# Kernel optimization log

Measured on AMD Instinct MI355X. Metric: run time of the kernel, lower is better.

The kernel has to match this reference:

```python
import jax, jax.numpy as jnp
import numpy as np

T, H, I, E, TOPK = 8192, 2048, 4096, 8, 2

def setup_inputs() -> dict:
    key = jax.random.key(0)
    k1, k2, k3, k4 = jax.random.split(key, 4)
    x = jax.random.normal(k1, (T, H), dtype=jnp.float32)
    gate_w = jax.random.normal(k2, (E, H), dtype=jnp.float32) * 0.02
    ws = jax.random.normal(k3, (E, 2 * I, H), dtype=jnp.float32) * 0.02
    w2s = jax.random.normal(k4, (E, H, I), dtype=jnp.float32) * 0.02
    return {"x": x, "gate_w": gate_w, "ws": ws, "w2s": w2s, "top_k": TOPK}

def reference(x, gate_w, ws, w2s, top_k):
    num_tokens = x.shape[0]
    num_experts = ws.shape[0]
    inter = w2s.shape[2]
    # --- router (fused_topk): softmax -> top-k -> renormalize ---
    logits = x @ gate_w.T                       # [T, E]
    probs = jax.nn.softmax(logits, axis=-1)
    topk_w, topk_ids = jax.lax.top_k(probs, top_k)   # [T, K]
    if top_k > 1:
        topk_w = topk_w / jnp.sum(topk_w, axis=-1, keepdims=True)
    # dense combine-weights [E, T]: sum of routing weights per (token, expert)
    tok = jnp.arange(num_tokens)
    cw = jnp.zeros((num_tokens, num_experts), dtype=x.dtype)
    cw = cw.at[tok[:, None], topk_ids].add(topk_w)
    cw = cw.T                                   # [E, T]
    # --- fused_experts: per-expert gated-SiLU MLP, weighted combine ---
    def body(acc, inp):
        e_ws, e_w2, e_cw = inp                  # [2I,H], [H,I], [T]
        gu = x @ e_ws.T                         # [T, 2I]
        g, u = gu[:, :inter], gu[:, inter:]
        h = jax.nn.silu(g) * u                  # SiluAndMul
        out = h @ e_w2.T                        # [T, H]
        return acc + e_cw[:, None] * out, None
    init = jnp.zeros_like(x)
    final, _ = jax.lax.scan(body, init, (ws, w2s, cw))
    return final
```

## Files before the change

kernel.cpp:

```cpp
#include <hip/hip_runtime.h>
#include <hip/hip_fp16.h>
#include <cstdint>
#include <cstddef>

#define TTOK 8192
#define HD   2048
#define ID   4096
#define NE   8
#define NPAIR (TTOK * 2)
#define PADROWS 18432
#define RBMAX 72

typedef _Float16 h8 __attribute__((ext_vector_type(8)));
typedef float    f4 __attribute__((ext_vector_type(4)));

#define VMWAIT(n) asm volatile("s_waitcnt vmcnt(" #n ")" ::: "memory")
#define MEMFENCE  asm volatile("" ::: "memory")
#define BAR()     __builtin_amdgcn_s_barrier()

__device__ __forceinline__ void async_cp16(const void* g, void* l) {
  __builtin_amdgcn_global_load_lds(
      (const __attribute__((address_space(1))) unsigned int*)g,
      (__attribute__((address_space(3))) unsigned int*)l, 16, 0, 0);
}

__device__ __forceinline__ f4 zero4() { f4 z = {0.f, 0.f, 0.f, 0.f}; return z; }

template <bool NT>
__global__ void cvt_kernel(const float* __restrict__ src, _Float16* __restrict__ dst, size_t n) {
  size_t stride = (size_t)gridDim.x * blockDim.x * 8;
  for (size_t i = ((size_t)blockIdx.x * blockDim.x + threadIdx.x) * 8; i < n; i += stride) {
    const float4* s = (const float4*)(src + i);
    float4 a = s[0], b = s[1];
    h8 o;
    o[0] = (_Float16)a.x; o[1] = (_Float16)a.y; o[2] = (_Float16)a.z; o[3] = (_Float16)a.w;
    o[4] = (_Float16)b.x; o[5] = (_Float16)b.y; o[6] = (_Float16)b.z; o[7] = (_Float16)b.w;
    if constexpr (NT) __builtin_nontemporal_store(o, (h8*)(dst + i));
    else *(h8*)(dst + i) = o;
  }
}

__device__ __forceinline__ void cvt_w2_half(const float* __restrict__ w2f,
                                            _Float16* __restrict__ dst,
                                            int kh, int cb, int ncb) {
  const size_t n = (size_t)NE * HD * 2048;
  size_t stride = (size_t)ncb * 512 * 8;
  for (size_t j = ((size_t)cb * 512 + threadIdx.x) * 8; j < n; j += stride) {
    size_t row = j >> 11, ic = j & 2047;
    const float4* s = (const float4*)(w2f + row * ID + (size_t)kh * 2048 + ic);
    float4 a = s[0], b = s[1];
    h8 o;
    o[0] = (_Float16)a.x; o[1] = (_Float16)a.y; o[2] = (_Float16)a.z; o[3] = (_Float16)a.w;
    o[4] = (_Float16)b.x; o[5] = (_Float16)b.y; o[6] = (_Float16)b.z; o[7] = (_Float16)b.w;
    *(h8*)(dst + row * 2048 + ic) = o;
  }
}

__global__ __launch_bounds__(512) void cvt_w2half_kernel(
    const float* __restrict__ w2f, _Float16* __restrict__ dst, int kh) {
  cvt_w2_half(w2f, dst, kh, blockIdx.x, gridDim.x);
}

__global__ __launch_bounds__(256) void gate_kernel(
    const float* __restrict__ x, const float* __restrict__ gw,
    int* __restrict__ counts, int* __restrict__ tids, float* __restrict__ tw,
    _Float16* __restrict__ xh) {
  int lane = threadIdx.x & 63;
  int t = blockIdx.x * 4 + (threadIdx.x >> 6);
  const float* xr = x + (size_t)t * HD;
  _Float16* xhr = xh + (size_t)t * HD;
  float acc[NE];
#pragma unroll
  for (int e = 0; e < NE; e++) acc[e] = 0.f;
  for (int j = lane; j < HD; j += 64) {
    float xv = xr[j];
    xhr[j] = (_Float16)xv;
#pragma unroll
    for (int e = 0; e < NE; e++) acc[e] += xv * gw[e * HD + j];
  }
#pragma unroll
  for (int off = 32; off > 0; off >>= 1) {
#pragma unroll
    for (int e = 0; e < NE; e++) acc[e] += __shfl_xor(acc[e], off, 64);
  }
  if (lane == 0) {
    int e0 = 0; float v0 = acc[0];
#pragma unroll
    for (int e = 1; e < NE; e++) if (acc[e] > v0) { v0 = acc[e]; e0 = e; }
    int e1 = -1; float v1 = -1e30f;
#pragma unroll
    for (int e = 0; e < NE; e++) if (e != e0 && acc[e] > v1) { v1 = acc[e]; e1 = e; }
    float b = __expf(v1 - v0);
    float w0 = 1.f / (1.f + b);
    tids[2 * t] = e0; tids[2 * t + 1] = e1;
    tw[2 * t] = w0;   tw[2 * t + 1] = b * w0;
    atomicAdd(&counts[e0], 1); atomicAdd(&counts[e1], 1);
  }
}

__global__ void scan_kernel(const int* __restrict__ counts, int* __restrict__ offs,
                            int* __restrict__ cursor) {
  if (threadIdx.x == 0 && blockIdx.x == 0) {
    int off = 0;
    for (int e = 0; e < NE; e++) {
      offs[e] = off; cursor[e] = off;
      off += ((counts[e] + 255) >> 8) << 8;
    }
    offs[NE] = off;
  }
}

__global__ void scatter_kernel(const int* __restrict__ tids, const float* __restrict__ tw,
                               int* __restrict__ cursor, int* __restrict__ perm,
                               float* __restrict__ pw, int* __restrict__ pairpos) {
  int t = blockIdx.x * 256 + threadIdx.x;
#pragma unroll
  for (int k = 0; k < 2; k++) {
    int e = tids[2 * t + k];
    int pos = atomicAdd(&cursor[e], 1);
    perm[pos] = t; pw[pos] = tw[2 * t + k];
    pairpos[2 * t + k] = pos;
  }
}

__global__ void padfill_kernel(const int* __restrict__ counts, const int* __restrict__ offs,
                               int* __restrict__ perm) {
  int s = blockIdx.x * 256 + threadIdx.x;
#pragma unroll
  for (int e = 0; e < NE; e++) {
    if (s >= offs[e] + counts[e] && s < offs[e + 1]) perm[s] = -1;
  }
}

#define LA(BB, H) ((BB) * 65536 + (H) * 16384)
#define LB(BB, H) ((BB) * 65536 + 32768 + (H) * 16384)
#define RD(boff) (*(const h8*)(smem + (boff)))

#define LOAD_AF(BB, MH) do { \
  af[0][0] = RD(LA(BB,MH) + amoff + 0*2048 + sa0); \
  af[0][1] = RD(LA(BB,MH) + amoff + 0*2048 + sa1); \
  af[1][0] = RD(LA(BB,MH) + amoff + 1*2048 + sa0); \
  af[1][1] = RD(LA(BB,MH) + amoff + 1*2048 + sa1); \
  af[2][0] = RD(LA(BB,MH) + amoff + 2*2048 + sa0); \
  af[2][1] = RD(LA(BB,MH) + amoff + 2*2048 + sa1); \
  af[3][0] = RD(LA(BB,MH) + amoff + 3*2048 + sa0); \
  af[3][1] = RD(LA(BB,MH) + amoff + 3*2048 + sa1); } while (0)

#define LOAD_BFG(BB) do { \
  bfg[0][0] = RD(LB(BB,0) + bnoff + 0*2048 + sa0); \
  bfg[0][1] = RD(LB(BB,0) + bnoff + 0*2048 + sa1); \
  bfg[1][0] = RD(LB(BB,0) + bnoff + 1*2048 + sa0); \
  bfg[1][1] = RD(LB(BB,0) + bnoff + 1*2048 + sa1); } while (0)

#define LOAD_BFU(BB) do { \
  bfu[0][0] = RD(LB(BB,1) + bnoff + 0*2048 + sa0); \
  bfu[0][1] = RD(LB(BB,1) + bnoff + 0*2048 + sa1); \
  bfu[1][0] = RD(LB(BB,1) + bnoff + 1*2048 + sa0); \
  bfu[1][1] = RD(LB(BB,1) + bnoff + 1*2048 + sa1); } while (0)

#define MM(MH,NH,BF,M,N) \
  acc[MH][NH][M][N] = __builtin_amdgcn_mfma_f32_16x16x32_f16(af[M][0], BF[N][0], acc[MH][NH][M][N], 0, 0, 0); \
  acc[MH][NH][M][N] = __builtin_amdgcn_mfma_f32_16x16x32_f16(af[M][1], BF[N][1], acc[MH][NH][M][N], 0, 0, 0);

#define MFMAQ(MH,NH,BF) do { __builtin_amdgcn_s_setprio(1); \
  MM(MH,NH,BF,0,0) MM(MH,NH,BF,0,1) MM(MH,NH,BF,1,0) MM(MH,NH,BF,1,1) \
  MM(MH,NH,BF,2,0) MM(MH,NH,BF,2,1) MM(MH,NH,BF,3,0) MM(MH,NH,BF,3,1) \
  __builtin_amdgcn_s_setprio(0); } while (0)

#define STG(gp, ldsbyte, kt) do { \
  async_cp16(gp[0] + (size_t)(kt) * 64, smem + (ldsbyte) + (wid * 2 + 0) * 1024 + lane * 16); \
  async_cp16(gp[1] + (size_t)(kt) * 64, smem + (ldsbyte) + (wid * 2 + 1) * 1024 + lane * 16); } while (0)

#define ACC_ZERO() do { \
  _Pragma("unroll") for (int mh = 0; mh < 2; mh++) \
  _Pragma("unroll") for (int nh = 0; nh < 2; nh++) \
  _Pragma("unroll") for (int m = 0; m < 4; m++) \
  _Pragma("unroll") for (int n = 0; n < 2; n++) acc[mh][nh][m][n] = zero4(); } while (0)

#define KLOOP(NI) \
  STG(gA[0], LA(0,0), 0); STG(gA[1], LA(0,1), 0); \
  STG(gB[0], LB(0,0), 0); STG(gB[1], LB(0,1), 0); \
  STG(gA[0], LA(1,0), 1); STG(gB[1], LB(1,1), 1); \
  VMWAIT(4); \
  BAR(); \
  for (int i = 0; i < (NI); ++i) { \
    bool last = (i == (NI) - 1); \
    int kt1 = 2 * i + 1, kt2 = 2 * i + 2, kt3 = 2 * i + 3; \
     \
    MEMFENCE; LOAD_AF(0,0); LOAD_BFG(0); \
    STG(gA[1], LA(1,1), kt1); STG(gB[0], LB(1,0), kt1); \
    BAR(); MEMFENCE; MFMAQ(0,0,bfg); BAR(); \
     \
    MEMFENCE; LOAD_BFU(0); \
    BAR(); MEMFENCE; MFMAQ(0,1,bfu); BAR(); \
     \
    MEMFENCE; LOAD_AF(0,1); \
    if (!last) STG(gA[0], LA(0,0), kt2); \
    BAR(); MEMFENCE; MFMAQ(1,1,bfu); BAR(); \
     \
    MEMFENCE; \
    if (!last) { STG(gB[1], LB(0,1), kt2); VMWAIT(4); } else { VMWAIT(0); } \
    BAR(); MEMFENCE; MFMAQ(1,0,bfg); BAR(); \
     \
    MEMFENCE; LOAD_AF(1,0); LOAD_BFG(1); \
    if (!last) { STG(gA[1], LA(0,1), kt2); STG(gB[0], LB(0,0), kt2); } \
    BAR(); MEMFENCE; MFMAQ(0,0,bfg); BAR(); \
     \
    MEMFENCE; LOAD_BFU(1); \
    BAR(); MEMFENCE; MFMAQ(0,1,bfu); BAR(); \
     \
    MEMFENCE; LOAD_AF(1,1); \
    if (!last) STG(gA[0], LA(1,0), kt3); \
    BAR(); MEMFENCE; MFMAQ(1,1,bfu); BAR(); \
     \
    MEMFENCE; \
    if (!last) { STG(gB[1], LB(1,1), kt3); VMWAIT(4); } \
    BAR(); MEMFENCE; MFMAQ(1,0,bfg); BAR(); \
  }

__device__ __forceinline__ int expert_of(const int* offs, int row0) {
  int e = 0;
#pragma unroll
  for (int k = 1; k < NE; k++) if (offs[k] <= row0) e = k;
  return e;
}

__global__ __launch_bounds__(512, 2) void gemm1_kernel(
    const _Float16* __restrict__ xh, const _Float16* __restrict__ wsh,
    const int* __restrict__ offs, const int* __restrict__ perm,
    _Float16* __restrict__ hb,
    const float* __restrict__ w2f, _Float16* __restrict__ w2h0) {
  int bx = blockIdx.x, gyy = blockIdx.y;
  if (gyy >= RBMAX) {
    cvt_w2_half(w2f, w2h0, 0, (gyy - RBMAX) * 32 + bx, 256);
    return;
  }
  int row0 = gyy << 8;
  if (row0 >= offs[NE]) return;
  int e = expert_of(offs, row0);
  int n0 = bx << 7;

  __shared__ char smem[131072];
  int tid = threadIdx.x, lane = tid & 63, wid = tid >> 6;
  int wm = wid >> 2, wn = wid & 3;
  int lr = lane & 15, ks = lane >> 4;
  int sa0 = lr * 128 + (((ks)     ^ (lr & 7)) << 4);
  int sa1 = lr * 128 + (((ks + 4) ^ (lr & 7)) << 4);
  int amoff = wm * 8192;
  int bnoff = wn * 4096;

  int srow = wid * 16 + (lane >> 3);
  int scol = ((lane & 7) ^ (lane >> 3)) * 8;
  const _Float16* gA[2][2]; const _Float16* gB[2][2];
#pragma unroll
  for (int h = 0; h < 2; h++)
#pragma unroll
    for (int j = 0; j < 2; j++) {
      int r = row0 + h * 128 + srow + j * 8;
      int pv = perm[r]; if (pv < 0) pv = 0;
      gA[h][j] = xh + (size_t)pv * HD + scol;
      gB[h][j] = wsh + ((size_t)e * 2 * ID + (size_t)h * ID + n0 + srow + j * 8) * HD + scol;
    }

  f4 acc[2][2][4][2];
  h8 af[4][2], bfg[2][2], bfu[2][2];
  ACC_ZERO();

  KLOOP(16)

#pragma unroll
  for (int mh = 0; mh < 2; mh++)
#pragma unroll
    for (int m = 0; m < 4; m++)
#pragma unroll
      for (int n = 0; n < 2; n++)
#pragma unroll
        for (int r = 0; r < 4; r++) {
          float g = acc[mh][0][m][n][r], u = acc[mh][1][m][n][r];
          float hv = g / (1.f + __expf(-g)) * u;
          int row = row0 + mh * 128 + wm * 64 + m * 16 + ks * 4 + r;
          int col = n0 + wn * 32 + n * 16 + lr;
          __builtin_nontemporal_store((_Float16)hv, hb + (size_t)row * ID + col);
        }
}

__global__ __launch_bounds__(512, 2) void gemm2_kernel(
    const _Float16* __restrict__ hb, const _Float16* __restrict__ w2h0,
    const _Float16* __restrict__ w2h1, const int* __restrict__ offs,
    _Float16* __restrict__ hb2) {
  int bx = blockIdx.x, gyy = blockIdx.y;
  int row0 = gyy << 8;
  if (row0 >= offs[NE]) return;
  int e = expert_of(offs, row0);
  int n0 = bx << 8;
  int kh = blockIdx.z;
  const _Float16* w2hk = kh ? w2h1 : w2h0;
  size_t k0 = (size_t)kh * 2048;

  __shared__ char smem[131072];
  int tid = threadIdx.x, lane = tid & 63, wid = tid >> 6;
  int wm = wid >> 2, wn = wid & 3;
  int lr = lane & 15, ks = lane >> 4;
  int sa0 = lr * 128 + (((ks)     ^ (lr & 7)) << 4);
  int sa1 = lr * 128 + (((ks + 4) ^ (lr & 7)) << 4);
  int amoff = wm * 8192;
  int bnoff = wn * 4096;

  int srow = wid * 16 + (lane >> 3);
  int scol = ((lane & 7) ^ (lane >> 3)) * 8;
  const _Float16* gA[2][2]; const _Float16* gB[2][2];
#pragma unroll
  for (int h = 0; h < 2; h++)
#pragma unroll
    for (int j = 0; j < 2; j++) {
      gA[h][j] = hb + ((size_t)(row0 + h * 128 + srow + j * 8)) * ID + k0 + scol;
      gB[h][j] = w2hk + ((size_t)e * HD + n0 + h * 128 + srow + j * 8) * 2048 + scol;
    }

  f4 acc[2][2][4][2];
  h8 af[4][2], bfg[2][2], bfu[2][2];
  ACC_ZERO();

  KLOOP(16)

  _Float16* dst = hb2 + (size_t)kh * PADROWS * HD;
#pragma unroll
  for (int mh = 0; mh < 2; mh++)
#pragma unroll
    for (int nh = 0; nh < 2; nh++)
#pragma unroll
      for (int m = 0; m < 4; m++)
#pragma unroll
        for (int n = 0; n < 2; n++)
#pragma unroll
          for (int r = 0; r < 4; r++) {
            int row = row0 + mh * 128 + wm * 64 + m * 16 + ks * 4 + r;
            int col = n0 + nh * 128 + wn * 32 + n * 16 + lr;
            hb2[(size_t)kh * PADROWS * HD + (size_t)row * HD + col] =
                (_Float16)acc[mh][nh][m][n][r];
            (void)dst;
          }
}

__global__ __launch_bounds__(256) void combine_kernel(
    const _Float16* __restrict__ hb2, const int* __restrict__ pairpos,
    const float* __restrict__ pw, float* __restrict__ out) {
  int i = blockIdx.x * 256 + threadIdx.x;
  int t = i >> 8, g = (i & 255) * 8;
  int p0 = pairpos[2 * t], p1 = pairpos[2 * t + 1];
  float w0 = pw[p0], w1 = pw[p1];
  const _Float16* hb2b = hb2 + (size_t)PADROWS * HD;
  h8 a0 = *(const h8*)(hb2  + (size_t)p0 * HD + g);
  h8 a1 = *(const h8*)(hb2b + (size_t)p0 * HD + g);
  h8 b0 = *(const h8*)(hb2  + (size_t)p1 * HD + g);
  h8 b1 = *(const h8*)(hb2b + (size_t)p1 * HD + g);
  f4 o0, o1;
#pragma unroll
  for (int j = 0; j < 4; j++)
    o0[j] = w0 * ((float)a0[j] + (float)a1[j]) + w1 * ((float)b0[j] + (float)b1[j]);
#pragma unroll
  for (int j = 0; j < 4; j++)
    o1[j] = w0 * ((float)a0[j + 4] + (float)a1[j + 4]) + w1 * ((float)b0[j + 4] + (float)b1[j + 4]);
  __builtin_nontemporal_store(o0, (f4*)(out + (size_t)t * HD + g));
  __builtin_nontemporal_store(o1, (f4*)(out + (size_t)t * HD + g + 4));
}

extern "C" void kernel_launch(void* const* d_in, const int* in_sizes, int n_in,
                              void* d_out, int out_size, void* d_ws, size_t ws_size,
                              hipStream_t stream) {
  const float* x   = (const float*)d_in[0];
  const float* gw  = (const float*)d_in[1];
  const float* wsf = (const float*)d_in[2];
  const float* w2f = (const float*)d_in[3];

  int* counts   = (int*)d_ws;
  int* offs     = counts + 8;
  int* cursor   = offs + 16;
  int* tids     = cursor + 8;
  float* tw     = (float*)(tids + NPAIR);
  int* perm     = (int*)(tw + NPAIR);
  float* pw     = (float*)(perm + PADROWS);
  int* pairpos  = (int*)(pw + PADROWS);

  char* base = (char*)d_ws;
  size_t off_xh   = (size_t)512 * 1024;
  size_t off_hb   = off_xh + (size_t)TTOK * HD * 2;
  size_t off_w2h0 = off_hb + (size_t)PADROWS * ID * 2;
  size_t off_big  = off_w2h0 + (size_t)NE * HD * 2048 * 2;
  size_t need     = off_big + (size_t)NE * 2 * ID * HD * 2;
  if (ws_size < need) return;

  _Float16* xh   = (_Float16*)(base + off_xh);
  _Float16* hb   = (_Float16*)(base + off_hb);
  _Float16* w2h0 = (_Float16*)(base + off_w2h0);
  _Float16* wsh  = (_Float16*)(base + off_big);
  _Float16* w2h1 = (_Float16*)(base + off_big);
  _Float16* hb2  = (_Float16*)(base + off_big + (size_t)NE * HD * 2048 * 2);

  hipMemsetAsync(counts, 0, 64, stream);

  cvt_kernel<false><<<4096, 256, 0, stream>>>(wsf, wsh, (size_t)NE * 2 * ID * HD);
  gate_kernel<<<TTOK / 4, 256, 0, stream>>>(x, gw, counts, tids, tw, xh);
  scan_kernel<<<1, 64, 0, stream>>>(counts, offs, cursor);
  scatter_kernel<<<TTOK / 256, 256, 0, stream>>>(tids, tw, cursor, perm, pw, pairpos);
  padfill_kernel<<<PADROWS / 256, 256, 0, stream>>>(counts, offs, perm);

  gemm1_kernel<<<dim3(ID / 128, RBMAX + 8), 512, 0, stream>>>(
      xh, wsh, offs, perm, hb, w2f, w2h0);

  cvt_w2half_kernel<<<512, 512, 0, stream>>>(w2f, w2h1, 1);

  gemm2_kernel<<<dim3(HD / 256, RBMAX, 2), 512, 0, stream>>>(
      hb, w2h0, w2h1, offs, hb2);

  combine_kernel<<<(TTOK * HD / 8) / 256, 256, 0, stream>>>(
      hb2, pairpos, pw, (float*)d_out);
}
```

Baseline: 1.389 ms.

## Split gemm1 into per-expert-pair launches overlapping weight conversion

Replaces the monolithic fp32→fp16 conversion of all expert gate/up weights with a small upfront conversion of experts 0-1. gemm1 is then launched four times, each handling one expert pair, while an extra block row converts the next pair's weights and slices of w2. The goal is to hide the large weight-conversion traffic behind GEMM compute instead of running it serially before gemm1. The cost is three more launches and smaller per-launch grids that may underfill the GPU, with conversion blocks competing for bandwidth.

```diff
diff --git a/kernel.cpp b/kernel.cpp
--- a/kernel.cpp
+++ b/kernel.cpp
@@ -10,6 +10,7 @@
 #define NPAIR (TTOK * 2)
 #define PADROWS 18432
 #define RBMAX 72
+#define WS_SLAB ((size_t)2 * ID * HD)
 
 typedef _Float16 h8 __attribute__((ext_vector_type(8)));
 typedef float    f4 __attribute__((ext_vector_type(4)));
@@ -26,17 +27,17 @@
 
 __device__ __forceinline__ f4 zero4() { f4 z = {0.f, 0.f, 0.f, 0.f}; return z; }
 
-template <bool NT>
-__global__ void cvt_kernel(const float* __restrict__ src, _Float16* __restrict__ dst, size_t n) {
-  size_t stride = (size_t)gridDim.x * blockDim.x * 8;
-  for (size_t i = ((size_t)blockIdx.x * blockDim.x + threadIdx.x) * 8; i < n; i += stride) {
-    const float4* s = (const float4*)(src + i);
+__device__ __forceinline__ void cvt_slice(const float* __restrict__ src,
+                                          _Float16* __restrict__ dst,
+                                          size_t base, size_t n, int cb, int ncb) {
+  size_t stride = (size_t)ncb * 512 * 8;
+  for (size_t i = ((size_t)cb * 512 + threadIdx.x) * 8; i < n; i += stride) {
+    const float4* s = (const float4*)(src + base + i);
     float4 a = s[0], b = s[1];
     h8 o;
     o[0] = (_Float16)a.x; o[1] = (_Float16)a.y; o[2] = (_Float16)a.z; o[3] = (_Float16)a.w;
     o[4] = (_Float16)b.x; o[5] = (_Float16)b.y; o[6] = (_Float16)b.z; o[7] = (_Float16)b.w;
-    if constexpr (NT) __builtin_nontemporal_store(o, (h8*)(dst + i));
-    else *(h8*)(dst + i) = o;
+    *(h8*)(dst + base + i) = o;
   }
 }
 
@@ -56,9 +57,9 @@
   }
 }
 
-__global__ __launch_bounds__(512) void cvt_w2half_kernel(
-    const float* __restrict__ w2f, _Float16* __restrict__ dst, int kh) {
-  cvt_w2_half(w2f, dst, kh, blockIdx.x, gridDim.x);
+__global__ __launch_bounds__(512) void cvt_ws01_kernel(
+    const float* __restrict__ wsf, _Float16* __restrict__ wsh) {
+  cvt_slice(wsf, wsh, 0, 2 * WS_SLAB, blockIdx.x, gridDim.x);
 }
 
 __global__ __launch_bounds__(256) void gate_kernel(
@@ -229,14 +230,19 @@
     const _Float16* __restrict__ xh, const _Float16* __restrict__ wsh,
     const int* __restrict__ offs, const int* __restrict__ perm,
     _Float16* __restrict__ hb,
-    const float* __restrict__ w2f, _Float16* __restrict__ w2h0) {
-  int bx = blockIdx.x, gyy = blockIdx.y;
-  if (gyy >= RBMAX) {
-    cvt_w2_half(w2f, w2h0, 0, (gyy - RBMAX) * 32 + bx, 256);
+    const float* __restrict__ wsf, const float* __restrict__ w2f,
+    _Float16* __restrict__ w2h0, _Float16* __restrict__ w2h1, int pid) {
+  if (blockIdx.y == 0) {
+    int tb = blockIdx.x;
+    if (pid < 3)
+      cvt_slice(wsf, (_Float16*)wsh, (size_t)(2 * pid + 2) * WS_SLAB, 2 * WS_SLAB, tb, 32);
+    if (pid < 2) cvt_w2_half(w2f, w2h0, 0, pid * 32 + tb, 64);
+    else         cvt_w2_half(w2f, w2h1, 1, (pid - 2) * 32 + tb, 64);
     return;
   }
+  int bx = blockIdx.x, gyy = blockIdx.y - 1;
   int row0 = gyy << 8;
-  if (row0 >= offs[NE]) return;
+  if (row0 < offs[2 * pid] || row0 >= offs[2 * pid + 2]) return;
   int e = expert_of(offs, row0);
   int n0 = bx << 7;
 
@@ -323,7 +329,6 @@
 
   KLOOP(16)
 
-  _Float16* dst = hb2 + (size_t)kh * PADROWS * HD;
 #pragma unroll
   for (int mh = 0; mh < 2; mh++)
 #pragma unroll
@@ -338,7 +343,6 @@
             int col = n0 + nh * 128 + wn * 32 + n * 16 + lr;
             hb2[(size_t)kh * PADROWS * HD + (size_t)row * HD + col] =
                 (_Float16)acc[mh][nh][m][n][r];
-            (void)dst;
           }
 }
 
@@ -399,16 +403,15 @@
 
   hipMemsetAsync(counts, 0, 64, stream);
 
-  cvt_kernel<false><<<4096, 256, 0, stream>>>(wsf, wsh, (size_t)NE * 2 * ID * HD);
   gate_kernel<<<TTOK / 4, 256, 0, stream>>>(x, gw, counts, tids, tw, xh);
+  cvt_ws01_kernel<<<256, 512, 0, stream>>>(wsf, wsh);
   scan_kernel<<<1, 64, 0, stream>>>(counts, offs, cursor);
   scatter_kernel<<<TTOK / 256, 256, 0, stream>>>(tids, tw, cursor, perm, pw, pairpos);
   padfill_kernel<<<PADROWS / 256, 256, 0, stream>>>(counts, offs, perm);
 
-  gemm1_kernel<<<dim3(ID / 128, RBMAX + 8), 512, 0, stream>>>(
-      xh, wsh, offs, perm, hb, w2f, w2h0);
-
-  cvt_w2half_kernel<<<512, 512, 0, stream>>>(w2f, w2h1, 1);
+  for (int pid = 0; pid < 4; ++pid)
+    gemm1_kernel<<<dim3(32, RBMAX + 1), 512, 0, stream>>>(
+        xh, wsh, offs, perm, hb, wsf, w2f, w2h0, w2h1, pid);
 
   gemm2_kernel<<<dim3(HD / 256, RBMAX, 2), 512, 0, stream>>>(
       hb, w2h0, w2h1, offs, hb2);
```

Result: slower. 1.598 ms (+15.0%).
